# Kernel optimization log

Measured on AMD Instinct MI355X. Metric: run time of the kernel, lower is better.

The kernel has to match this reference:

```python
import jax, jax.numpy as jnp
import numpy as np

DIM = 1024
N_HEADS = 16
HEAD_DIM = DIM // N_HEADS
COND_DIM = 1024
MLP_RATIO = 4
B, S = 4, 1024
LN_EPS = 1e-5


def _layer_norm(x, w):
    # F.layer_norm without affine bias, then * weight (per original LayerNorm)
    x32 = x.astype(jnp.float32)
    mu = jnp.mean(x32, axis=-1, keepdims=True)
    var = jnp.var(x32, axis=-1, keepdims=True)
    return (x32 - mu) * jax.lax.rsqrt(var + LN_EPS) * w


def _rope(t, cos, sin):
    # t: [b, s, h, d]; cos/sin: [s, d/2]; rotate-half convention
    d2 = t.shape[-1] // 2
    t1, t2 = t[..., :d2], t[..., d2:]
    c = cos[None, :, None, :]
    s = sin[None, :, None, :]
    return jnp.concatenate([t1 * c - t2 * s, t2 * c + t1 * s], axis=-1)


def setup_inputs() -> dict:
    key = jax.random.key(0)
    ks = jax.random.split(key, 12)
    inv_freq = 1.0 / (10000.0 ** (np.arange(0, HEAD_DIM, 2) / HEAD_DIM))
    ang = np.arange(S)[:, None] * inv_freq[None, :]
    return {
        "x": jax.random.normal(ks[0], (B, S, DIM), jnp.float32),
        "cos": jnp.asarray(np.cos(ang), jnp.float32),
        "sin": jnp.asarray(np.sin(ang), jnp.float32),
        "c": jax.random.normal(ks[1], (B, COND_DIM), jnp.float32),
        "w_ln1": jnp.ones((DIM,), jnp.float32),
        "w_ln2": jnp.ones((DIM,), jnp.float32),
        "w_qkv": jax.random.normal(ks[2], (DIM, 3 * DIM), jnp.float32) * 0.02,
        "w_attn_out": jax.random.normal(ks[3], (DIM, DIM), jnp.float32) * 0.02,
        "w_mlp1": jax.random.normal(ks[4], (DIM, MLP_RATIO * DIM), jnp.float32) * 0.02,
        "b_mlp1": jnp.zeros((MLP_RATIO * DIM,), jnp.float32),
        "w_mlp2": jax.random.normal(ks[5], (MLP_RATIO * DIM, DIM), jnp.float32) * 0.02,
        "b_mlp2": jnp.zeros((DIM,), jnp.float32),
        "w_ada": jax.random.normal(ks[6], (COND_DIM, 6 * DIM), jnp.float32) * 0.02,
        "b_ada": jax.random.normal(ks[7], (6 * DIM,), jnp.float32) * 0.02,
    }


def reference(x, cos, sin, c, w_ln1, w_ln2, w_qkv, w_attn_out,
              w_mlp1, b_mlp1, w_mlp2, b_mlp2, w_ada, b_ada):
    b, s, dim = x.shape
    # adaLN modulation: [b, 6*dim] -> six [b, 1, dim] chunks
    mod = (c @ w_ada + b_ada)[:, None, :]
    shift_msa, scale_msa, gate_msa, shift_mlp, scale_mlp, gate_mlp = jnp.split(mod, 6, axis=2)

    x_skip = x
    h = _layer_norm(x, w_ln1) * (1.0 + scale_msa) + shift_msa
    qkv = (h @ w_qkv).reshape(b, s, 3, N_HEADS, HEAD_DIM)
    q = _rope(qkv[:, :, 0], cos, sin)
    k = _rope(qkv[:, :, 1], cos, sin)
    v = qkv[:, :, 2]

    scale = 1.0 / jnp.sqrt(jnp.asarray(HEAD_DIM, x.dtype))
    scores = jnp.einsum('bshd,bthd->bhst', q, k) * scale  # [b,h,s,s]
    attn = jax.nn.softmax(scores, axis=-1)
    o = jnp.einsum('bhst,bthd->bshd', attn, v).reshape(b, s, dim)

    x = x_skip + gate_msa * (o @ w_attn_out)

    h2 = _layer_norm(x, w_ln2) * (1.0 + scale_mlp) + shift_mlp
    m = jax.nn.gelu(h2 @ w_mlp1 + b_mlp1, approximate=True) @ w_mlp2 + b_mlp2
    return x + gate_mlp * m
```

## Files before the change

### kernel.cpp

```cpp
#include <hip/hip_runtime.h>
#include <stdint.h>

typedef unsigned short u16;
typedef __bf16 bf16x8 __attribute__((ext_vector_type(8)));
typedef float f32x4 __attribute__((ext_vector_type(4)));

#define MOD6  6144

__device__ __forceinline__ float b2f(unsigned int u) {
    union { unsigned int i; float f; } z; z.i = u << 16; return z.f;
}
__device__ __forceinline__ u16 f2b(float f) {
    union { float f; unsigned int i; } z; z.f = f;
    unsigned int i = z.i;
    return (u16)((i + 0x7fffu + ((i >> 16) & 1u)) >> 16);
}
union U4 { uint4 u; u16 s[8]; };
union U2 { uint2 u; u16 s[4]; };
union B8 { bf16x8 v; unsigned int w[4]; };

__device__ __forceinline__ float ldf(const void* p, size_t i, int isbf) {
    if (isbf) return b2f(((const u16*)p)[i]);
    return ((const float*)p)[i];
}
__device__ __forceinline__ void load4(const void* p, size_t i, int isbf, float* v) {
    if (isbf) {
        U2 t; t.u = *(const uint2*)((const u16*)p + i);
#pragma unroll
        for (int e = 0; e < 4; e++) v[e] = b2f(t.s[e]);
    } else {
        float4 f = *(const float4*)((const float*)p + i);
        v[0] = f.x; v[1] = f.y; v[2] = f.z; v[3] = f.w;
    }
}

__device__ __forceinline__ void gld16(u16* lds, const u16* g) {
    __builtin_amdgcn_global_load_lds(
        (__attribute__((address_space(1))) void*)(g),
        (__attribute__((address_space(3))) void*)(lds), 16, 0, 0);
}

__global__ void detect_dtype(const unsigned int* __restrict__ w, int* __restrict__ flag) {
    if (threadIdx.x == 0 && blockIdx.x == 0)
        *flag = (w[0] == 0x3F803F80u) ? 1 : 0;
}

__global__ void transpose_any(const void* __restrict__ in, u16* __restrict__ out,
                              int K, int N, const int* __restrict__ flag) {
    const int isbf = *flag;
    __shared__ u16 tile[64][66];
    const int ntn = N >> 6;
    const int k0 = (blockIdx.x / ntn) << 6;
    const int n0 = (blockIdx.x % ntn) << 6;
    const int tid = threadIdx.x;
    const int r = tid >> 3;
    const int c = (tid & 7) * 8;
#pragma unroll
    for (int rr = 0; rr < 64; rr += 32) {
        const size_t base = (size_t)(k0 + r + rr) * N + n0 + c;
        u16* t = &tile[r + rr][c];
        if (isbf) {
            U4 v; v.u = *(const uint4*)((const u16*)in + base);
#pragma unroll
            for (int e = 0; e < 8; e++) t[e] = v.s[e];
        } else {
            float4 a = *(const float4*)((const float*)in + base);
            float4 b = *(const float4*)((const float*)in + base + 4);
            t[0] = f2b(a.x); t[1] = f2b(a.y); t[2] = f2b(a.z); t[3] = f2b(a.w);
            t[4] = f2b(b.x); t[5] = f2b(b.y); t[6] = f2b(b.z); t[7] = f2b(b.w);
        }
    }
    __syncthreads();
#pragma unroll
    for (int rr = 0; rr < 64; rr += 32) {
        U4 v;
#pragma unroll
        for (int e = 0; e < 8; e++) v.s[e] = tile[c + e][r + rr];
        *(uint4*)&out[(size_t)(n0 + r + rr) * K + k0 + c] = v.u;
    }
}

__global__ void ada_partial(const void* __restrict__ c, const void* __restrict__ w_ada,
                            float* __restrict__ part, const int* __restrict__ flag) {
    const int isbf = *flag;
    const int g = blockIdx.x * 256 + threadIdx.x;
    const int slice = g / 24576;
    const int idx = g - slice * 24576;
    const int b = idx / MOD6, n = idx - (idx / MOD6) * MOD6;
    const int k0 = slice * 128;
    float acc = 0.f;
    if (isbf) {
        const u16* cr = (const u16*)c + b * 1024 + k0;
        const u16* wp = (const u16*)w_ada + (size_t)k0 * MOD6 + n;
#pragma unroll 8
        for (int k = 0; k < 128; k++)
            acc += b2f(cr[k]) * b2f(wp[(size_t)k * MOD6]);
    } else {
        const float* cr = (const float*)c + b * 1024 + k0;
        const float* wp = (const float*)w_ada + (size_t)k0 * MOD6 + n;
#pragma unroll 8
        for (int k = 0; k < 128; k++)
            acc += cr[k] * wp[(size_t)k * MOD6];
    }
    part[g] = acc;
}
__global__ void ada_reduce(const float* __restrict__ part, const void* __restrict__ b_ada,
                           float* __restrict__ mod, const int* __restrict__ flag) {
    const int g = blockIdx.x * 256 + threadIdx.x;
    float acc = ldf(b_ada, g % MOD6, *flag);
#pragma unroll
    for (int s = 0; s < 8; s++) acc += part[s * 24576 + g];
    mod[g] = acc;
}

__global__ void ln_mod_kernel(const void* __restrict__ x, const void* __restrict__ w,
                              const float* __restrict__ mod, int shift_off,
                              int scale_off, u16* __restrict__ out,
                              const int* __restrict__ flag, int x_is_f32) {
    const int isbf = *flag;
    const int xb = x_is_f32 ? 0 : isbf;
    const int tk = blockIdx.x;
    const int b = tk >> 10;
    const int tid = threadIdx.x;
    float v[4];
    load4(x, (size_t)tk * 1024 + tid * 4, xb, v);
    float s = v[0] + v[1] + v[2] + v[3];
    float ss = v[0]*v[0] + v[1]*v[1] + v[2]*v[2] + v[3]*v[3];
#pragma unroll
    for (int off = 1; off < 64; off <<= 1) {
        s  += __shfl_xor(s, off);
        ss += __shfl_xor(ss, off);
    }
    __shared__ float ls[4], lss[4];
    if ((tid & 63) == 0) { ls[tid >> 6] = s; lss[tid >> 6] = ss; }
    __syncthreads();
    s  = ls[0] + ls[1] + ls[2] + ls[3];
    ss = lss[0] + lss[1] + lss[2] + lss[3];
    const float mu  = s * (1.f / 1024.f);
    const float var = ss * (1.f / 1024.f) - mu * mu;
    const float rstd = rsqrtf(var + 1e-5f);
    float wv[4];
    load4(w, (size_t)tid * 4, isbf, wv);
    const float* mb = mod + (size_t)b * MOD6;
    U2 o;
#pragma unroll
    for (int e = 0; e < 4; e++) {
        const int col = tid * 4 + e;
        float n = (v[e] - mu) * rstd * wv[e];
        o.s[e] = f2b(n * (1.f + mb[scale_off + col]) + mb[shift_off + col]);
    }
    *(uint2*)(out + (size_t)tk * 1024 + tid * 4) = o.u;
}

#define EPI_STORE 0
#define EPI_RES_GATE 1
#define EPI_GELU_BIAS 2
#define EPI_RES_GATE_BIAS 3

template <int EPI>
__launch_bounds__(256, 2)
__global__ void gemm_bt(const u16* __restrict__ A, const u16* __restrict__ Bt,
                        void* __restrict__ Cv, int M, int N, int K,
                        const void* __restrict__ res, const float* __restrict__ gate,
                        const void* __restrict__ bias, const int* __restrict__ flag) {
    __shared__ __align__(16) u16 sA[128 * 32];
    __shared__ __align__(16) u16 sB[128 * 32];
    const int isbf = flag ? *flag : 0;
    const int tid = threadIdx.x;
    const int lane = tid & 63;
    const int w = tid >> 6;
    const int wm = w >> 1, wn = w & 1;
    const int c16 = lane & 15, quad = lane >> 4;
    const int m0 = blockIdx.y * 128, n0 = blockIdx.x * 128;

    const int srow = lane >> 2;
    const int schunk = lane & 3;
    const int gchunk = schunk ^ (srow & 3);

    const u16* gA = A + (size_t)m0 * K + 8 * gchunk;
    const u16* gB = Bt + (size_t)n0 * K + 8 * gchunk;
    const int cs = quad ^ (c16 & 3);

    f32x4 acc[4][4];
#pragma unroll
    for (int i = 0; i < 4; i++)
#pragma unroll
        for (int j = 0; j < 4; j++) acc[i][j] = (f32x4){0.f, 0.f, 0.f, 0.f};

#pragma unroll 1
    for (int kt = 0; kt < K; kt += 32) {
        __syncthreads();
#pragma unroll
        for (int p = 0; p < 2; p++) {
            const int r = 16 * (w + 4 * p) + srow;
            gld16(&sA[r * 32 + 8 * schunk], gA + (size_t)r * K + kt);
            gld16(&sB[r * 32 + 8 * schunk], gB + (size_t)r * K + kt);
        }
        __syncthreads();
        bf16x8 af[4], bfr[4];
#pragma unroll
        for (int i = 0; i < 4; i++)
            af[i] = *(const bf16x8*)&sA[(64 * wm + 16 * i + c16) * 32 + 8 * cs];
#pragma unroll
        for (int j = 0; j < 4; j++)
            bfr[j] = *(const bf16x8*)&sB[(64 * wn + 16 * j + c16) * 32 + 8 * cs];
#pragma unroll
        for (int i = 0; i < 4; i++)
#pragma unroll
            for (int j = 0; j < 4; j++)
                acc[i][j] = __builtin_amdgcn_mfma_f32_16x16x32_bf16(
                    af[i], bfr[j], acc[i][j], 0, 0, 0);
    }

#pragma unroll
    for (int i = 0; i < 4; i++) {
#pragma unroll
        for (int r = 0; r < 4; r++) {
            const int row = m0 + 64 * wm + 16 * i + 4 * quad + r;
            const int b = row >> 10;
#pragma unroll
            for (int j = 0; j < 4; j++) {
                const int col = n0 + 64 * wn + 16 * j + c16;
                float v = acc[i][j][r];
                if constexpr (EPI == EPI_GELU_BIAS) {
                    v += ldf(bias, col, isbf);
                    const float u = 0.7978845608f * (v + 0.044715f * v * v * v);
                    const float e = __expf(2.f * u);
                    const float t = 1.f - 2.f / (e + 1.f);
                    v = 0.5f * v * (1.f + t);
                } else if constexpr (EPI == EPI_RES_GATE) {
                    v = ldf(res, (size_t)row * N + col, isbf)
                        + gate[(size_t)b * MOD6 + col] * v;
                } else if constexpr (EPI == EPI_RES_GATE_BIAS) {
                    v += ldf(bias, col, isbf);
                    v = ((const float*)res)[(size_t)row * N + col]
                        + gate[(size_t)b * MOD6 + col] * v;
                }
                if constexpr (EPI == EPI_RES_GATE || EPI == EPI_RES_GATE_BIAS) {
                    ((float*)Cv)[(size_t)row * N + col] = v;
                } else {
                    ((u16*)Cv)[(size_t)row * N + col] = f2b(v);
                }
            }
        }
    }
}

__global__ void rope_kernel(u16* __restrict__ qkv, const void* __restrict__ cosb,
                            const void* __restrict__ sinb, const int* __restrict__ flag) {
    const int isbf = *flag;
    const int g = blockIdx.x * 256 + threadIdx.x;
    const int q8 = g & 7;
    const int h = (g >> 3) & 15;
    const int tk = g >> 7;
    const int s = tk & 1023;
    const int d = q8 * 4;
    u16* row = qkv + (size_t)tk * 3072;

    float c4[4], s4[4];
    load4(cosb, (size_t)s * 32 + d, isbf, c4);
    load4(sinb, (size_t)s * 32 + d, isbf, s4);

#pragma unroll
    for (int which = 0; which < 2; which++) {
        u16* p1 = row + which * 1024 + h * 64 + d;
        u16* p2 = p1 + 32;
        U2 t1, t2;
        t1.u = *(const uint2*)p1;
        t2.u = *(const uint2*)p2;
        U2 o1, o2;
#pragma unroll
        for (int e = 0; e < 4; e++) {
            const float a = b2f(t1.s[e]), bb = b2f(t2.s[e]);
            o1.s[e] = f2b(a * c4[e] - bb * s4[e]);
            o2.s[e] = f2b(bb * c4[e] + a * s4[e]);
        }
        *(uint2*)p1 = o1.u;
        *(uint2*)p2 = o2.u;
    }
}

__launch_bounds__(256, 4)
__global__ void attn_mfma(const u16* __restrict__ qkv, u16* __restrict__ o_out) {
    __shared__ __align__(16) u16 sK[64 * 72];
    __shared__ __align__(16) u16 sVt[64 * 72];
    const int bh = blockIdx.x >> 4;
    const int qt = blockIdx.x & 15;
    const int b = bh >> 4, h = bh & 15;
    const int tid = threadIdx.x;
    const int w = tid >> 6;
    const int lane = tid & 63;
    const int c = lane & 15;
    const int quad = lane >> 4;

    const int q0 = qt * 64 + w * 16;
    bf16x8 qf0, qf1;
    {
        const u16* qrow = qkv + (size_t)(b * 1024 + q0 + c) * 3072 + h * 64;
        qf0 = *(const bf16x8*)(qrow + quad * 8);
        qf1 = *(const bf16x8*)(qrow + 32 + quad * 8);
    }
    f32x4 of[4];
#pragma unroll
    for (int dt = 0; dt < 4; dt++) of[dt] = (f32x4){0.f, 0.f, 0.f, 0.f};
    float mI = -1e30f, lI = 0.f;

    const int skey = tid >> 3;
    const int sch  = tid & 7;
    const int src0 = (((2 * quad) & 3) << 4) + c;
    const int src1 = (((2 * quad + 1) & 3) << 4) + c;

#pragma unroll 1
    for (int kt = 0; kt < 1024; kt += 64) {
        __syncthreads();
#pragma unroll
        for (int p = 0; p < 2; p++) {
            const int key = skey + p * 32;
            const u16* krow = qkv + (size_t)(b * 1024 + kt + key) * 3072 + 1024
                              + h * 64 + sch * 8;
            uint4 kv = *(const uint4*)krow;
            *(uint4*)&sK[key * 72 + sch * 8] = kv;
            U4 vv; vv.u = *(const uint4*)(krow + 1024);
#pragma unroll
            for (int e = 0; e < 8; e++) sVt[(sch * 8 + e) * 72 + key] = vv.s[e];
        }
        __syncthreads();
#pragma unroll
        for (int ks = 0; ks < 64; ks += 32) {
            bf16x8 k00 = *(const bf16x8*)&sK[(ks + c) * 72 + quad * 8];
            bf16x8 k01 = *(const bf16x8*)&sK[(ks + c) * 72 + 32 + quad * 8];
            bf16x8 k10 = *(const bf16x8*)&sK[(ks + 16 + c) * 72 + quad * 8];
            bf16x8 k11 = *(const bf16x8*)&sK[(ks + 16 + c) * 72 + 32 + quad * 8];
            f32x4 s0 = (f32x4){0.f, 0.f, 0.f, 0.f};
            f32x4 s1 = (f32x4){0.f, 0.f, 0.f, 0.f};
            s0 = __builtin_amdgcn_mfma_f32_16x16x32_bf16(k00, qf0, s0, 0, 0, 0);
            s0 = __builtin_amdgcn_mfma_f32_16x16x32_bf16(k01, qf1, s0, 0, 0, 0);
            s1 = __builtin_amdgcn_mfma_f32_16x16x32_bf16(k10, qf0, s1, 0, 0, 0);
            s1 = __builtin_amdgcn_mfma_f32_16x16x32_bf16(k11, qf1, s1, 0, 0, 0);
            float sc[8];
#pragma unroll
            for (int r = 0; r < 4; r++) { sc[r] = s0[r] * 0.125f; sc[4 + r] = s1[r] * 0.125f; }
            float tm = sc[0];
#pragma unroll
            for (int j = 1; j < 8; j++) tm = fmaxf(tm, sc[j]);
            tm = fmaxf(tm, __shfl_xor(tm, 16));
            tm = fmaxf(tm, __shfl_xor(tm, 32));
            const float mNew = fmaxf(mI, tm);
            const float alpha = __expf(mI - mNew);
            float p8[8];
            float psum = 0.f;
#pragma unroll
            for (int j = 0; j < 8; j++) { p8[j] = __expf(sc[j] - mNew); psum += p8[j]; }
            psum += __shfl_xor(psum, 16);
            psum += __shfl_xor(psum, 32);
            lI = lI * alpha + psum;
            mI = mNew;
#pragma unroll
            for (int dt = 0; dt < 4; dt++) {
#pragma unroll
                for (int r = 0; r < 4; r++) of[dt][r] *= alpha;
            }
            const unsigned int a0 = (unsigned)f2b(p8[0]) | ((unsigned)f2b(p8[1]) << 16);
            const unsigned int a1 = (unsigned)f2b(p8[2]) | ((unsigned)f2b(p8[3]) << 16);
            const unsigned int b0 = (unsigned)f2b(p8[4]) | ((unsigned)f2b(p8[5]) << 16);
            const unsigned int b1 = (unsigned)f2b(p8[6]) | ((unsigned)f2b(p8[7]) << 16);
            const unsigned int xa0 = (unsigned)__shfl((int)a0, src0);
            const unsigned int xb0 = (unsigned)__shfl((int)b0, src0);
            const unsigned int xa1 = (unsigned)__shfl((int)a1, src0);
            const unsigned int xb1 = (unsigned)__shfl((int)b1, src0);
            const unsigned int ya0 = (unsigned)__shfl((int)a0, src1);
            const unsigned int yb0 = (unsigned)__shfl((int)b0, src1);
            const unsigned int ya1 = (unsigned)__shfl((int)a1, src1);
            const unsigned int yb1 = (unsigned)__shfl((int)b1, src1);
            B8 pf;
            pf.w[0] = quad < 2 ? xa0 : xb0;
            pf.w[1] = quad < 2 ? xa1 : xb1;
            pf.w[2] = quad < 2 ? ya0 : yb0;
            pf.w[3] = quad < 2 ? ya1 : yb1;
#pragma unroll
            for (int dt = 0; dt < 4; dt++) {
                bf16x8 vf = *(const bf16x8*)&sVt[(dt * 16 + c) * 72 + ks + quad * 8];
                of[dt] = __builtin_amdgcn_mfma_f32_16x16x32_bf16(vf, pf.v, of[dt], 0, 0, 0);
            }
        }
    }
    const float inv = 1.f / lI;
    const size_t orow = (size_t)(b * 1024 + q0 + c) * 1024 + h * 64;
#pragma unroll
    for (int dt = 0; dt < 4; dt++) {
        U2 pk;
#pragma unroll
        for (int r = 0; r < 4; r++) pk.s[r] = f2b(of[dt][r] * inv);
        *(uint2*)(o_out + orow + dt * 16 + quad * 4) = pk.u;
    }
}

extern "C" void kernel_launch(void* const* d_in, const int* in_sizes, int n_in,
                              void* d_out, int out_size, void* d_ws, size_t ws_size,
                              hipStream_t stream) {
    (void)in_sizes; (void)n_in; (void)out_size; (void)ws_size;
    const void* x      = d_in[0];
    const void* cosb   = d_in[1];
    const void* sinb   = d_in[2];
    const void* c      = d_in[3];
    const void* w_ln1  = d_in[4];
    const void* w_ln2  = d_in[5];
    const void* w_qkv  = d_in[6];
    const void* w_attn = d_in[7];
    const void* w_mlp1 = d_in[8];
    const void* b_mlp1 = d_in[9];
    const void* w_mlp2 = d_in[10];
    const void* b_mlp2 = d_in[11];
    const void* w_ada  = d_in[12];
    const void* b_ada  = d_in[13];
    char* ws = (char*)d_ws;

    u16*   wT_qkv  = (u16*)(ws + 0);
    u16*   wT_attn = (u16*)(ws + 6291456);
    u16*   wT_mlp1 = (u16*)(ws + 8388608);
    u16*   wT_mlp2 = (u16*)(ws + 16777216);
    float* mod     = (float*)(ws + 25165824);
    u16*   hbuf    = (u16*)(ws + 25264128);
    u16*   big     = (u16*)(ws + 33652736);
    float* x2      = (float*)(ws + 67207168);
    int*   flag    = (int*)(ws + 83984384);
    float* part    = (float*)big;

    detect_dtype<<<1, 64, 0, stream>>>((const unsigned int*)w_ln1, flag);
    transpose_any<<<dim3(16 * 48), 256, 0, stream>>>(w_qkv, wT_qkv, 1024, 3072, flag);
    transpose_any<<<dim3(16 * 16), 256, 0, stream>>>(w_attn, wT_attn, 1024, 1024, flag);
    transpose_any<<<dim3(16 * 64), 256, 0, stream>>>(w_mlp1, wT_mlp1, 1024, 4096, flag);
    transpose_any<<<dim3(64 * 16), 256, 0, stream>>>(w_mlp2, wT_mlp2, 4096, 1024, flag);
    ada_partial<<<768, 256, 0, stream>>>(c, w_ada, part, flag);
    ada_reduce<<<96, 256, 0, stream>>>(part, b_ada, mod, flag);
    ln_mod_kernel<<<4096, 256, 0, stream>>>(x, w_ln1, mod, 0, 1024, hbuf, flag, 0);
    gemm_bt<EPI_STORE><<<dim3(24, 32), 256, 0, stream>>>(
        hbuf, wT_qkv, big, 4096, 3072, 1024, nullptr, nullptr, nullptr, flag);
    rope_kernel<<<2048, 256, 0, stream>>>(big, cosb, sinb, flag);
    attn_mfma<<<1024, 256, 0, stream>>>(big, hbuf);
    gemm_bt<EPI_RES_GATE><<<dim3(8, 32), 256, 0, stream>>>(
        hbuf, wT_attn, x2, 4096, 1024, 1024, x, mod + 2048, nullptr, flag);
    ln_mod_kernel<<<4096, 256, 0, stream>>>(x2, w_ln2, mod, 3072, 4096, hbuf, flag, 1);
    gemm_bt<EPI_GELU_BIAS><<<dim3(32, 32), 256, 0, stream>>>(
        hbuf, wT_mlp1, big, 4096, 4096, 1024, nullptr, nullptr, b_mlp1, flag);
    gemm_bt<EPI_RES_GATE_BIAS><<<dim3(8, 32), 256, 0, stream>>>(
        big, wT_mlp2, (float*)d_out, 4096, 1024, 4096, x2, mod + 5120, b_mlp2, flag);
}
```

Measured before the change: 468.8 us.

## Split-K the MLP down-projection GEMM with atomic accumulation into output

The final MLP2 GEMM (K=4096) launched only 256 blocks. It now splits K into four slices across blockIdx.z, giving 1024 blocks, and accumulates gate-scaled partial products into the output with float atomicAdd. A new out_init kernel first writes the residual plus the gated bias into the output. The aim is to fill the GPU better in a long-K GEMM, at the cost of an extra elementwise pass, atomic traffic and non-deterministic summation order.

```diff
diff --git a/kernel.cpp b/kernel.cpp
--- a/kernel.cpp
+++ b/kernel.cpp
@@ -152,17 +152,39 @@
     *(uint2*)(out + (size_t)tk * 1024 + tid * 4) = o.u;
 }
 
+__global__ void out_init(const float* __restrict__ res, const float* __restrict__ gate,
+                         const void* __restrict__ bias, float* __restrict__ out,
+                         const int* __restrict__ flag) {
+    const int isbf = *flag;
+    const int g = blockIdx.x * 256 + threadIdx.x;
+    const int col = (g & 255) * 4;
+    const int row = g >> 8;
+    const int b = row >> 10;
+    float bv[4];
+    load4(bias, (size_t)col, isbf, bv);
+    const float* gp = gate + (size_t)b * MOD6 + col;
+    float4 r = *(const float4*)(res + (size_t)row * 1024 + col);
+    float4 o;
+    o.x = r.x + gp[0] * bv[0];
+    o.y = r.y + gp[1] * bv[1];
+    o.z = r.z + gp[2] * bv[2];
+    o.w = r.w + gp[3] * bv[3];
+    *(float4*)(out + (size_t)row * 1024 + col) = o;
+}
+
 #define EPI_STORE 0
 #define EPI_RES_GATE 1
 #define EPI_GELU_BIAS 2
 #define EPI_RES_GATE_BIAS 3
+#define EPI_ATOMIC_GATE 4
 
 template <int EPI>
 __launch_bounds__(256, 2)
 __global__ void gemm_bt(const u16* __restrict__ A, const u16* __restrict__ Bt,
                         void* __restrict__ Cv, int M, int N, int K,
                         const void* __restrict__ res, const float* __restrict__ gate,
-                        const void* __restrict__ bias, const int* __restrict__ flag) {
+                        const void* __restrict__ bias, const int* __restrict__ flag,
+                        int Ks) {
     __shared__ __align__(16) u16 sA[128 * 32];
     __shared__ __align__(16) u16 sB[128 * 32];
     const int isbf = flag ? *flag : 0;
@@ -172,6 +194,7 @@
     const int wm = w >> 1, wn = w & 1;
     const int c16 = lane & 15, quad = lane >> 4;
     const int m0 = blockIdx.y * 128, n0 = blockIdx.x * 128;
+    const int kt0 = blockIdx.z * Ks;
 
     const int srow = lane >> 2;
     const int schunk = lane & 3;
@@ -188,7 +211,7 @@
         for (int j = 0; j < 4; j++) acc[i][j] = (f32x4){0.f, 0.f, 0.f, 0.f};
 
 #pragma unroll 1
-    for (int kt = 0; kt < K; kt += 32) {
+    for (int kt = kt0; kt < kt0 + Ks; kt += 32) {
         __syncthreads();
 #pragma unroll
         for (int p = 0; p < 2; p++) {
@@ -236,7 +259,10 @@
                     v = ((const float*)res)[(size_t)row * N + col]
                         + gate[(size_t)b * MOD6 + col] * v;
                 }
-                if constexpr (EPI == EPI_RES_GATE || EPI == EPI_RES_GATE_BIAS) {
+                if constexpr (EPI == EPI_ATOMIC_GATE) {
+                    atomicAdd((float*)Cv + (size_t)row * N + col,
+                              gate[(size_t)b * MOD6 + col] * v);
+                } else if constexpr (EPI == EPI_RES_GATE || EPI == EPI_RES_GATE_BIAS) {
                     ((float*)Cv)[(size_t)row * N + col] = v;
                 } else {
                     ((u16*)Cv)[(size_t)row * N + col] = f2b(v);
@@ -435,14 +461,16 @@
     ada_reduce<<<96, 256, 0, stream>>>(part, b_ada, mod, flag);
     ln_mod_kernel<<<4096, 256, 0, stream>>>(x, w_ln1, mod, 0, 1024, hbuf, flag, 0);
     gemm_bt<EPI_STORE><<<dim3(24, 32), 256, 0, stream>>>(
-        hbuf, wT_qkv, big, 4096, 3072, 1024, nullptr, nullptr, nullptr, flag);
+        hbuf, wT_qkv, big, 4096, 3072, 1024, nullptr, nullptr, nullptr, flag, 1024);
     rope_kernel<<<2048, 256, 0, stream>>>(big, cosb, sinb, flag);
     attn_mfma<<<1024, 256, 0, stream>>>(big, hbuf);
     gemm_bt<EPI_RES_GATE><<<dim3(8, 32), 256, 0, stream>>>(
-        hbuf, wT_attn, x2, 4096, 1024, 1024, x, mod + 2048, nullptr, flag);
+        hbuf, wT_attn, x2, 4096, 1024, 1024, x, mod + 2048, nullptr, flag, 1024);
     ln_mod_kernel<<<4096, 256, 0, stream>>>(x2, w_ln2, mod, 3072, 4096, hbuf, flag, 1);
+    out_init<<<4096, 256, 0, stream>>>(x2, mod + 5120, b_mlp2, (float*)d_out, flag);
     gemm_bt<EPI_GELU_BIAS><<<dim3(32, 32), 256, 0, stream>>>(
-        hbuf, wT_mlp1, big, 4096, 4096, 1024, nullptr, nullptr, b_mlp1, flag);
-    gemm_bt<EPI_RES_GATE_BIAS><<<dim3(8, 32), 256, 0, stream>>>(
-        big, wT_mlp2, (float*)d_out, 4096, 1024, 4096, x2, mod + 5120, b_mlp2, flag);
-}
+        hbuf, wT_mlp1, big, 4096, 4096, 1024, nullptr, nullptr, b_mlp1, flag, 1024);
+    gemm_bt<EPI_ATOMIC_GATE><<<dim3(8, 32, 4), 256, 0, stream>>>(
+        big, wT_mlp2, (float*)d_out, 4096, 1024, 4096, nullptr, mod + 5120, nullptr,
+        flag, 1024);
+}
```

New measurement: 474.3 us. Within noise of the previous version (+1.2%).
